# Kernel tuning notes

Measured on AMD Instinct MI355X. Metric: run time of the kernel, lower is better.

The kernel has to match this reference:

```python
import jax, jax.numpy as jnp
import numpy as np
from jax import lax

# Static configuration (torch module passes these as shape lists / init kwargs)
RATE = 2
FUSE_K = 3
SOFTMAX_SCALE = 10.0
B, L, C = 1, 4096, 64
HS = WS = 64            # downscaled foreground spatial (int_fs)
HB = WB = 64            # background patch grid (int_bs); HB*WB == L
KP = 2 * RATE           # raw patch kernel size = 4
PAD_T = 1               # torch conv_transpose2d padding


def setup_inputs() -> dict:
    key = jax.random.key(0)
    ks = jax.random.split(key, 6)
    raw_w = jax.random.normal(ks[0], (B, L, C, KP, KP), jnp.float32) * 0.1
    mm = (jax.random.uniform(ks[1], (B, L, 1, 1)) > 0.5).astype(jnp.float32)
    scores = jax.random.normal(ks[2], (B, L, HS, WS), jnp.float32)
    w1 = jax.random.normal(ks[3], (C, C, 3, 3), jnp.float32) * 0.05
    b1 = jnp.zeros((C,), jnp.float32)
    w2 = jax.random.normal(ks[4], (C, C, 3, 3), jnp.float32) * 0.05
    b2 = jnp.zeros((C,), jnp.float32)
    return {"raw_w": raw_w, "mm": mm, "scores": scores,
            "w1": w1, "b1": b1, "w2": w2, "b2": b2}


def _conv2d(x, w, b=None, padding=1):
    y = lax.conv_general_dilated(x, w, (1, 1), [(padding, padding)] * 2,
                                 dimension_numbers=('NCHW', 'OIHW', 'NCHW'))
    if b is not None:
        y = y + b[None, :, None, None]
    return y


def _fuse(yi):
    # Diagonal-kernel fusion (DeepFill): treat scores as a (HB*WB) x (HS*WS) image
    # and convolve with an identity (eye) kernel along both pairings.
    k = FUSE_K
    eye = jnp.eye(k, dtype=yi.dtype)[None, None]  # [1,1,k,k]
    x = yi.reshape(B, 1, HB * WB, HS * WS)
    x = _conv2d(x, eye, padding=k // 2)
    x = x.reshape(B, HB, WB, HS, WS).transpose(0, 2, 1, 4, 3)
    x = x.reshape(B, 1, WB * HB, WS * HS)
    x = _conv2d(x, eye, padding=k // 2)
    x = x.reshape(B, WB, HB, WS, HS).transpose(0, 2, 1, 4, 3)  # [B,HB,WB,HS,WS]
    return x.reshape(B, L, HS, WS)


def _deconv_item(y_b, w_b):
    # torch F.conv_transpose2d(y, w, stride=RATE, padding=PAD_T) for one item.
    # y_b: [L,HS,WS], w_b: [L,C,KP,KP] -> [C, RATE*HS, RATE*WS]
    wt = jnp.flip(w_b, axis=(-2, -1)).transpose(1, 0, 2, 3)  # [C,L,KP,KP]
    pad = KP - 1 - PAD_T
    out = lax.conv_general_dilated(y_b[None], wt, (1, 1), [(pad, pad)] * 2,
                                   lhs_dilation=(RATE, RATE),
                                   dimension_numbers=('NCHW', 'OIHW', 'NCHW'))
    return out[0] / 4.0  # overlap normalization (4 = number of overlapping patches)


def reference(raw_w, mm, scores, w1, b1, w2, b2):
    yi = _fuse(scores)
    yi = jax.nn.softmax(yi * mm * SOFTMAX_SCALE, axis=1) * mm  # softmax over L patches
    y = jax.vmap(_deconv_item)(yi, raw_w)  # [B, C, RATE*HS, RATE*WS]
    # trailing Conv+ELU x2 (self.out)
    y = jax.nn.elu(_conv2d(y, w1, b1))
    y = jax.nn.elu(_conv2d(y, w2, b2))
    return y
```

## Files before the change

kernel.cpp:

```cpp
#include <hip/hip_runtime.h>
#include <hip/hip_bf16.h>
#include <math.h>

#define NL 4096
#define NQ 4096
#define SCALE 10.0f

typedef __bf16 bf16x8 __attribute__((ext_vector_type(8)));
typedef float  f32x4  __attribute__((ext_vector_type(4)));
typedef float  f32x4u __attribute__((ext_vector_type(4), aligned(4)));

#define GLOAD_LDS16(gp, lp)                                                        \
    __builtin_amdgcn_global_load_lds((const __attribute__((address_space(1))) void*)(gp), \
                                     (__attribute__((address_space(3))) void*)(lp), \
                                     16, 0, 0)

__device__ __forceinline__ void ldtap(const float* __restrict__ S, int r, int c0,
                                      float t[4]) {
    if (r < 0 || r >= 4096) { t[0] = t[1] = t[2] = t[3] = 0.f; return; }
    const float* p = S + (size_t)r * 4096;
    if (c0 >= 0 && c0 <= 4092) {
        f32x4u v = *(const f32x4u*)(p + c0);
        t[0] = v.x; t[1] = v.y; t[2] = v.z; t[3] = v.w;
    } else {
        #pragma unroll
        for (int i = 0; i < 4; ++i) {
            int c = c0 + i;
            t[i] = (c >= 0 && c < 4096) ? p[c] : 0.f;
        }
    }
}

__global__ __launch_bounds__(256) void fuseD(const float* __restrict__ S,
                                             float* __restrict__ F) {
    int l = blockIdx.x;
    int hb = l >> 6, wb = l & 63;
    int rowb[3]; bool rok[3];
    #pragma unroll
    for (int d = 0; d < 3; ++d) {
        int h2 = hb + d - 1;
        if (h2 >= 0 && h2 <= 63) { rowb[d] = h2 * 64 + wb; rok[d] = true; }
        else if (h2 < 0)         { rowb[d] = 4031 + wb;    rok[d] = (wb >= 1); }
        else                     { rowb[d] = 1 + wb;       rok[d] = (wb <= 62); }
    }
    float* Fr = F + (size_t)l * 4096;

    #pragma unroll
    for (int cc = 0; cc < 4; ++cc) {
        int q0 = (cc * 256 + threadIdx.x) * 4;
        int hs = q0 >> 6, ws0 = q0 & 63;
        float acc[4] = {0.f, 0.f, 0.f, 0.f};
        #pragma unroll
        for (int d = 0; d < 3; ++d) {
            if (!rok[d]) continue;
            int s2 = hs + d - 1;
            int colb; float m0 = 1.f, m3 = 1.f;
            if (s2 >= 0 && s2 <= 63) colb = s2 * 64 + ws0;
            else if (s2 < 0) { colb = 4031 + ws0; if (ws0 == 0)  m0 = 0.f; }
            else             { colb = 1 + ws0;    if (ws0 == 60) m3 = 0.f; }
            float s3[4] = {0.f, 0.f, 0.f, 0.f};
            #pragma unroll
            for (int d1 = -1; d1 <= 1; ++d1) {
                float t[4];
                ldtap(S, rowb[d] + d1, colb + d1, t);
                s3[0] += t[0]; s3[1] += t[1]; s3[2] += t[2]; s3[3] += t[3];
            }
            acc[0] += m0 * s3[0]; acc[1] += s3[1]; acc[2] += s3[2]; acc[3] += m3 * s3[3];
        }
        *(float4*)&Fr[q0] = make_float4(acc[0], acc[1], acc[2], acc[3]);
    }
}

__global__ __launch_bounds__(256) void softPart(const float* __restrict__ F,
                                                const float* __restrict__ mm,
                                                float* __restrict__ Pm,
                                                float* __restrict__ Ps) {
    int qt = blockIdx.x, lc = blockIdx.y;
    int qo = threadIdx.x & 63, lg = threadIdx.x >> 6;
    int q = qt * 64 + qo;
    __shared__ float red[4][64];

    float sv[32];
    float m = -1e30f;
    #pragma unroll
    for (int i = 0; i < 32; ++i) {
        int l = lc * 128 + i * 4 + lg;
        float s = F[(size_t)l * 4096 + q] * mm[l] * SCALE;
        sv[i] = s;
        m = fmaxf(m, s);
    }
    red[lg][qo] = m;
    __syncthreads();
    m = fmaxf(fmaxf(red[0][qo], red[1][qo]), fmaxf(red[2][qo], red[3][qo]));
    __syncthreads();

    float sum = 0.f;
    #pragma unroll
    for (int i = 0; i < 32; ++i) sum += __expf(sv[i] - m);
    red[lg][qo] = sum;
    __syncthreads();
    if (lg == 0) {
        sum = red[0][qo] + red[1][qo] + red[2][qo] + red[3][qo];
        Pm[lc * 4096 + q] = m;
        Ps[lc * 4096 + q] = sum;
    }
}

__global__ void softComb(const float* __restrict__ Pm, const float* __restrict__ Ps,
                         float* __restrict__ Qm, float* __restrict__ Qi) {
    int q = blockIdx.x * 256 + threadIdx.x;
    float M = -1e30f;
    #pragma unroll
    for (int i = 0; i < 32; ++i) M = fmaxf(M, Pm[i * 4096 + q]);
    float S = 0.f;
    #pragma unroll
    for (int i = 0; i < 32; ++i) S += Ps[i * 4096 + q] * __expf(Pm[i * 4096 + q] - M);
    Qm[q] = M;
    Qi[q] = 1.0f / S;
}

__global__ __launch_bounds__(256) void normTransP(const float* __restrict__ F,
                                                  const float* __restrict__ mm,
                                                  const float* __restrict__ Qm,
                                                  const float* __restrict__ Qi,
                                                  __hip_bfloat16* __restrict__ Pt) {
    __shared__ float T[64][65];
    int qt = blockIdx.x, lt = blockIdx.y;
    int c = threadIdx.x & 63;
    int q = qt * 64 + c;
    float qm = Qm[q], qi = Qi[q];
    #pragma unroll
    for (int p = 0; p < 16; ++p) {
        int r = p * 4 + (threadIdx.x >> 6);
        int l = lt * 64 + r;
        float mml = mm[l];
        float s = F[(size_t)l * 4096 + q] * mml * SCALE - qm;
        T[r][c] = mml * __expf(s) * qi;
    }
    __syncthreads();
    #pragma unroll
    for (int p = 0; p < 16; ++p) {
        int r = p * 4 + (threadIdx.x >> 6);
        Pt[(size_t)(qt * 64 + r) * 4096 + lt * 64 + c] = (__hip_bfloat16)T[c][r];
    }
}

__global__ __launch_bounds__(256) void transW(const float* __restrict__ Wsrc,
                                              __hip_bfloat16* __restrict__ Wt) {
    __shared__ float T[64][65];
    int nt = blockIdx.x, kt = blockIdx.y;
    int c = threadIdx.x & 63;
    #pragma unroll
    for (int p = 0; p < 16; ++p) {
        int r = p * 4 + (threadIdx.x >> 6);
        T[r][c] = Wsrc[(size_t)(kt * 64 + r) * 1024 + nt * 64 + c];
    }
    __syncthreads();
    #pragma unroll
    for (int p = 0; p < 16; ++p) {
        int r = p * 4 + (threadIdx.x >> 6);
        int n_new = (r & 15) * 64 + nt * 4 + (r >> 4);
        Wt[(size_t)n_new * 4096 + kt * 64 + c] = (__hip_bfloat16)T[c][r];
    }
}

__global__ void transWc(const float* __restrict__ Wsrc, __hip_bfloat16* __restrict__ Wd) {
    int t = blockIdx.x * 256 + threadIdx.x;
    int kyx = t >> 12;
    int co = (t >> 6) & 63;
    int ci = t & 63;
    Wd[t] = (__hip_bfloat16)Wsrc[co * 576 + ci * 9 + kyx];
}

__global__ __launch_bounds__(256) void gemmMfma(const __hip_bfloat16* __restrict__ Ab,
                                                const __hip_bfloat16* __restrict__ Bb,
                                                float* __restrict__ Cm) {
    __shared__ __align__(16) __hip_bfloat16 As[2][128][32];
    __shared__ __align__(16) __hip_bfloat16 Bs[2][64][32];
    int tid = threadIdx.x;
    int lane = tid & 63, w = tid >> 6;
    int bm0 = blockIdx.x * 128, bn0 = blockIdx.y * 64;
    int wm = (w >> 1) * 64, wn = (w & 1) * 32;

    int srowA = w * 32 + (lane >> 2);
    int srowB = w * 16 + (lane >> 2);
    int scol = (((lane & 3) ^ ((lane >> 3) & 3))) * 8;
    const __hip_bfloat16* ga0 = Ab + (size_t)(bm0 + srowA) * 4096 + scol;
    const __hip_bfloat16* ga1 = Ab + (size_t)(bm0 + srowA + 16) * 4096 + scol;
    const __hip_bfloat16* gb0 = Bb + (size_t)(bn0 + srowB) * 4096 + scol;

    f32x4 acc[4][2] = {};
    int fm = lane & 15;
    int fkz = (((lane >> 4) ^ ((lane >> 1) & 3))) * 8;

    GLOAD_LDS16(ga0, &As[0][w * 32][0]);
    GLOAD_LDS16(ga1, &As[0][w * 32 + 16][0]);
    GLOAD_LDS16(gb0, &Bs[0][w * 16][0]);
    __syncthreads();

    int buf = 0;
    for (int t = 0; t < 128; ++t) {
        if (t + 1 < 128) {
            int k0 = (t + 1) * 32;
            GLOAD_LDS16(ga0 + k0, &As[buf ^ 1][w * 32][0]);
            GLOAD_LDS16(ga1 + k0, &As[buf ^ 1][w * 32 + 16][0]);
            GLOAD_LDS16(gb0 + k0, &Bs[buf ^ 1][w * 16][0]);
        }
        bf16x8 af[4], bfr[2];
        #pragma unroll
        for (int i = 0; i < 4; ++i)
            af[i] = *(const bf16x8*)&As[buf][wm + i * 16 + fm][fkz];
        #pragma unroll
        for (int j = 0; j < 2; ++j)
            bfr[j] = *(const bf16x8*)&Bs[buf][wn + j * 16 + fm][fkz];
        #pragma unroll
        for (int i = 0; i < 4; ++i)
            #pragma unroll
            for (int j = 0; j < 2; ++j)
                acc[i][j] = __builtin_amdgcn_mfma_f32_16x16x32_bf16(af[i], bfr[j], acc[i][j], 0, 0, 0);
        __syncthreads();
        buf ^= 1;
    }

    #pragma unroll
    for (int i = 0; i < 4; ++i) {
        #pragma unroll
        for (int j = 0; j < 2; ++j) {
            int row = bm0 + wm + i * 16 + (lane >> 4) * 4;
            int col = bn0 + wn + j * 16 + (lane & 15);
            #pragma unroll
            for (int r = 0; r < 4; ++r)
                Cm[(size_t)(row + r) * 1024 + col] = acc[i][j][r];
        }
    }
}

__global__ void scatterD(const float* __restrict__ Mo, __hip_bfloat16* __restrict__ Xp) {
    int c = threadIdx.x & 63;
    int pix = blockIdx.x * 4 + (threadIdx.x >> 6);
    int ox = pix & 127, oy = pix >> 7;
    float acc = 0.f;
    #pragma unroll
    for (int ky = 0; ky < 4; ++ky) {
        int ty = oy + 1 - ky;
        if (ty & 1) continue;
        int iy = ty >> 1;
        if (iy < 0 || iy >= 64) continue;
        #pragma unroll
        for (int kx = 0; kx < 4; ++kx) {
            int txx = ox + 1 - kx;
            if (txx & 1) continue;
            int ix = txx >> 1;
            if (ix < 0 || ix >= 64) continue;
            acc += Mo[(size_t)(iy * 64 + ix) * 1024 + (ky * 4 + kx) * 64 + c];
        }
    }
    Xp[((size_t)(oy + 1) * 130 + ox + 1) * 64 + c] = (__hip_bfloat16)(acc * 0.25f);
}

template <int MODE>
__global__ __launch_bounds__(256) void convMfma(const __hip_bfloat16* __restrict__ Xp,
                                                const __hip_bfloat16* __restrict__ Wc,
                                                const float* __restrict__ Bi,
                                                __hip_bfloat16* __restrict__ Yp,
                                                float* __restrict__ Yo) {
    int tid = threadIdx.x, lane = tid & 63, w = tid >> 6;
    int y = blockIdx.x >> 1, x0 = (blockIdx.x & 1) * 64;
    int co0 = w * 16;
    int fl = lane & 15, fh = lane >> 4;

    bf16x8 wb[3][3][2];
    #pragma unroll
    for (int ky = 0; ky < 3; ++ky)
        #pragma unroll
        for (int kx = 0; kx < 3; ++kx)
            #pragma unroll
            for (int kc = 0; kc < 2; ++kc)
                wb[ky][kx][kc] = *(const bf16x8*)&Wc[(size_t)((ky * 3 + kx) * 64 + co0 + fl) * 64 + kc * 32 + fh * 8];

    f32x4 acc[4] = {};
    #pragma unroll
    for (int ky = 0; ky < 3; ++ky) {
        #pragma unroll
        for (int kx = 0; kx < 3; ++kx) {
            const __hip_bfloat16* xrow = Xp + ((size_t)(y + ky) * 130 + x0 + kx) * 64;
            #pragma unroll
            for (int kc = 0; kc < 2; ++kc) {
                #pragma unroll
                for (int mt = 0; mt < 4; ++mt) {
                    bf16x8 af = *(const bf16x8*)&xrow[(mt * 16 + fl) * 64 + kc * 32 + fh * 8];
                    acc[mt] = __builtin_amdgcn_mfma_f32_16x16x32_bf16(af, wb[ky][kx][kc], acc[mt], 0, 0, 0);
                }
            }
        }
    }

    float bias = Bi[co0 + fl];
    #pragma unroll
    for (int mt = 0; mt < 4; ++mt) {
        int xb = x0 + mt * 16 + fh * 4;
        if (MODE == 0) {
            #pragma unroll
            for (int r = 0; r < 4; ++r) {
                float v = acc[mt][r] + bias;
                v = v > 0.f ? v : expm1f(v);
                Yp[((size_t)(y + 1) * 130 + xb + r + 1) * 64 + co0 + fl] = (__hip_bfloat16)v;
            }
        } else {
            float4 o;
            float* op = (float*)&o;
            #pragma unroll
            for (int r = 0; r < 4; ++r) {
                float v = acc[mt][r] + bias;
                op[r] = v > 0.f ? v : expm1f(v);
            }
            *(float4*)&Yo[(size_t)(co0 + fl) * 16384 + y * 128 + xb] = o;
        }
    }
}

extern "C" void kernel_launch(void* const* d_in, const int* in_sizes, int n_in,
                              void* d_out, int out_size, void* d_ws, size_t ws_size,
                              hipStream_t stream) {
    const float* raw_w  = (const float*)d_in[0];
    const float* mm     = (const float*)d_in[1];
    const float* scores = (const float*)d_in[2];
    const float* w1     = (const float*)d_in[3];
    const float* b1     = (const float*)d_in[4];
    const float* w2     = (const float*)d_in[5];
    const float* b2     = (const float*)d_in[6];
    float* out = (float*)d_out;

    char* ws = (char*)d_ws;
    __hip_bfloat16* Pt  = (__hip_bfloat16*)ws;
    __hip_bfloat16* Wt  = (__hip_bfloat16*)(ws + (32ull << 20));
    float*          Pm  = (float*)(ws + (40ull << 20));
    float*          Ps  = (float*)(ws + (40ull << 20) + (512u << 10));
    float*          Qm  = (float*)(ws + (41ull << 20));
    float*          Qi  = (float*)(ws + (41ull << 20) + (64u << 10));
    __hip_bfloat16* Wc1 = (__hip_bfloat16*)(ws + (41ull << 20) + (256u << 10));
    __hip_bfloat16* Wc2 = (__hip_bfloat16*)(ws + (41ull << 20) + (384u << 10));
    float*          Mo  = (float*)(ws + (42ull << 20));
    __hip_bfloat16* Xp  = (__hip_bfloat16*)(ws + (58ull << 20));
    __hip_bfloat16* Y1p = (__hip_bfloat16*)(ws + (61ull << 20));
    float*          F   = (float*)(ws + (64ull << 20));

    const size_t XP_BYTES = 130ull * 130 * 64 * sizeof(__hip_bfloat16);

    fuseD<<<4096, 256, 0, stream>>>(scores, F);
    transW<<<dim3(16, 64), 256, 0, stream>>>(raw_w, Wt);
    transWc<<<144, 256, 0, stream>>>(w1, Wc1);
    transWc<<<144, 256, 0, stream>>>(w2, Wc2);
    softPart<<<dim3(64, 32), 256, 0, stream>>>(F, mm, Pm, Ps);
    softComb<<<16, 256, 0, stream>>>(Pm, Ps, Qm, Qi);
    normTransP<<<dim3(64, 64), 256, 0, stream>>>(F, mm, Qm, Qi, Pt);
    gemmMfma<<<dim3(32, 16), 256, 0, stream>>>(Pt, Wt, Mo);
    hipMemsetAsync(Xp, 0, XP_BYTES, stream);
    hipMemsetAsync(Y1p, 0, XP_BYTES, stream);
    scatterD<<<4096, 256, 0, stream>>>(Mo, Xp);
    convMfma<0><<<256, 256, 0, stream>>>(Xp, Wc1, b1, Y1p, nullptr);
    convMfma<1><<<256, 256, 0, stream>>>(Y1p, Wc2, b2, nullptr, out);
}
```

Measured before the change: 198.3 us.

## Split-K GEMM with larger 128x128 tiles and XCD-aware block remapping

The main GEMM changes from 128x64 tiles over the full K=4096 to 128x128 tiles with a two-way split-K. The two partial results go to separate buffers (the second reuses the F region, which is no longer needed), and scatterD sums them. Block indices are remapped so neighbouring tiles land on the same XCD for better L2 reuse, and fuseD gets the same remap. The intent is more reuse per block and a full 512-block grid, at the cost of extra fp32 partial writes and reads in scatterD.

After: 177.0 us. 10.8% less time.

```diff
diff --git a/kernel.cpp b/kernel.cpp
--- a/kernel.cpp
+++ b/kernel.cpp
@@ -33,7 +33,8 @@
 
 __global__ __launch_bounds__(256) void fuseD(const float* __restrict__ S,
                                              float* __restrict__ F) {
-    int l = blockIdx.x;
+    int lin = blockIdx.x;
+    int l = (lin & 7) * 512 + (lin >> 3);
     int hb = l >> 6, wb = l & 63;
     int rowb[3]; bool rok[3];
     #pragma unroll
@@ -172,51 +173,62 @@
     Wd[t] = (__hip_bfloat16)Wsrc[co * 576 + ci * 9 + kyx];
 }
 
-__global__ __launch_bounds__(256) void gemmMfma(const __hip_bfloat16* __restrict__ Ab,
-                                                const __hip_bfloat16* __restrict__ Bb,
-                                                float* __restrict__ Cm) {
+__global__ __launch_bounds__(256) void gemmMfmaK(const __hip_bfloat16* __restrict__ Ab,
+                                                 const __hip_bfloat16* __restrict__ Bb,
+                                                 float* __restrict__ C0,
+                                                 float* __restrict__ C1) {
     __shared__ __align__(16) __hip_bfloat16 As[2][128][32];
-    __shared__ __align__(16) __hip_bfloat16 Bs[2][64][32];
+    __shared__ __align__(16) __hip_bfloat16 Bs[2][128][32];
+    int lin = blockIdx.x;
+    int wid = (lin & 7) * 64 + (lin >> 3);
+    int bm = wid & 31;
+    int bn = (wid >> 5) & 7;
+    int bz = wid >> 8;
+    int bm0 = bm * 128, bn0 = bn * 128;
+    size_t kbase = (size_t)bz * 2048;
+    float* Cm = bz ? C1 : C0;
+
     int tid = threadIdx.x;
     int lane = tid & 63, w = tid >> 6;
-    int bm0 = blockIdx.x * 128, bn0 = blockIdx.y * 64;
-    int wm = (w >> 1) * 64, wn = (w & 1) * 32;
-
-    int srowA = w * 32 + (lane >> 2);
-    int srowB = w * 16 + (lane >> 2);
+    int wm = (w >> 1) * 64, wn = (w & 1) * 64;
+
+    int srow = w * 32 + (lane >> 2);
     int scol = (((lane & 3) ^ ((lane >> 3) & 3))) * 8;
-    const __hip_bfloat16* ga0 = Ab + (size_t)(bm0 + srowA) * 4096 + scol;
-    const __hip_bfloat16* ga1 = Ab + (size_t)(bm0 + srowA + 16) * 4096 + scol;
-    const __hip_bfloat16* gb0 = Bb + (size_t)(bn0 + srowB) * 4096 + scol;
-
-    f32x4 acc[4][2] = {};
+    const __hip_bfloat16* ga0 = Ab + (size_t)(bm0 + srow) * 4096 + kbase + scol;
+    const __hip_bfloat16* ga1 = Ab + (size_t)(bm0 + srow + 16) * 4096 + kbase + scol;
+    const __hip_bfloat16* gb0 = Bb + (size_t)(bn0 + srow) * 4096 + kbase + scol;
+    const __hip_bfloat16* gb1 = Bb + (size_t)(bn0 + srow + 16) * 4096 + kbase + scol;
+
+    f32x4 acc[4][4] = {};
     int fm = lane & 15;
     int fkz = (((lane >> 4) ^ ((lane >> 1) & 3))) * 8;
 
     GLOAD_LDS16(ga0, &As[0][w * 32][0]);
     GLOAD_LDS16(ga1, &As[0][w * 32 + 16][0]);
-    GLOAD_LDS16(gb0, &Bs[0][w * 16][0]);
+    GLOAD_LDS16(gb0, &Bs[0][w * 32][0]);
+    GLOAD_LDS16(gb1, &Bs[0][w * 32 + 16][0]);
     __syncthreads();
 
     int buf = 0;
-    for (int t = 0; t < 128; ++t) {
-        if (t + 1 < 128) {
+    for (int t = 0; t < 64; ++t) {
+        if (t + 1 < 64) {
             int k0 = (t + 1) * 32;
             GLOAD_LDS16(ga0 + k0, &As[buf ^ 1][w * 32][0]);
             GLOAD_LDS16(ga1 + k0, &As[buf ^ 1][w * 32 + 16][0]);
-            GLOAD_LDS16(gb0 + k0, &Bs[buf ^ 1][w * 16][0]);
-        }
-        bf16x8 af[4], bfr[2];
+            GLOAD_LDS16(gb0 + k0, &Bs[buf ^ 1][w * 32][0]);
+            GLOAD_LDS16(gb1 + k0, &Bs[buf ^ 1][w * 32 + 16][0]);
+        }
+        bf16x8 af[4], bfr[4];
         #pragma unroll
         for (int i = 0; i < 4; ++i)
             af[i] = *(const bf16x8*)&As[buf][wm + i * 16 + fm][fkz];
         #pragma unroll
-        for (int j = 0; j < 2; ++j)
+        for (int j = 0; j < 4; ++j)
             bfr[j] = *(const bf16x8*)&Bs[buf][wn + j * 16 + fm][fkz];
         #pragma unroll
         for (int i = 0; i < 4; ++i)
             #pragma unroll
-            for (int j = 0; j < 2; ++j)
+            for (int j = 0; j < 4; ++j)
                 acc[i][j] = __builtin_amdgcn_mfma_f32_16x16x32_bf16(af[i], bfr[j], acc[i][j], 0, 0, 0);
         __syncthreads();
         buf ^= 1;
@@ -225,7 +237,7 @@
     #pragma unroll
     for (int i = 0; i < 4; ++i) {
         #pragma unroll
-        for (int j = 0; j < 2; ++j) {
+        for (int j = 0; j < 4; ++j) {
             int row = bm0 + wm + i * 16 + (lane >> 4) * 4;
             int col = bn0 + wn + j * 16 + (lane & 15);
             #pragma unroll
@@ -235,7 +247,8 @@
     }
 }
 
-__global__ void scatterD(const float* __restrict__ Mo, __hip_bfloat16* __restrict__ Xp) {
+__global__ void scatterD(const float* __restrict__ Mo, const float* __restrict__ Mo2,
+                         __hip_bfloat16* __restrict__ Xp) {
     int c = threadIdx.x & 63;
     int pix = blockIdx.x * 4 + (threadIdx.x >> 6);
     int ox = pix & 127, oy = pix >> 7;
@@ -252,7 +265,8 @@
             if (txx & 1) continue;
             int ix = txx >> 1;
             if (ix < 0 || ix >= 64) continue;
-            acc += Mo[(size_t)(iy * 64 + ix) * 1024 + (ky * 4 + kx) * 64 + c];
+            size_t off = (size_t)(iy * 64 + ix) * 1024 + (ky * 4 + kx) * 64 + c;
+            acc += Mo[off] + Mo2[off];
         }
     }
     Xp[((size_t)(oy + 1) * 130 + ox + 1) * 64 + c] = (__hip_bfloat16)(acc * 0.25f);
@@ -344,6 +358,7 @@
     __hip_bfloat16* Xp  = (__hip_bfloat16*)(ws + (58ull << 20));
     __hip_bfloat16* Y1p = (__hip_bfloat16*)(ws + (61ull << 20));
     float*          F   = (float*)(ws + (64ull << 20));
+    float*          Mo2 = (float*)(ws + (64ull << 20));
 
     const size_t XP_BYTES = 130ull * 130 * 64 * sizeof(__hip_bfloat16);
 
@@ -354,10 +369,10 @@
     softPart<<<dim3(64, 32), 256, 0, stream>>>(F, mm, Pm, Ps);
     softComb<<<16, 256, 0, stream>>>(Pm, Ps, Qm, Qi);
     normTransP<<<dim3(64, 64), 256, 0, stream>>>(F, mm, Qm, Qi, Pt);
-    gemmMfma<<<dim3(32, 16), 256, 0, stream>>>(Pt, Wt, Mo);
+    gemmMfmaK<<<512, 256, 0, stream>>>(Pt, Wt, Mo, Mo2);
     hipMemsetAsync(Xp, 0, XP_BYTES, stream);
     hipMemsetAsync(Y1p, 0, XP_BYTES, stream);
-    scatterD<<<4096, 256, 0, stream>>>(Mo, Xp);
+    scatterD<<<4096, 256, 0, stream>>>(Mo, Mo2, Xp);
     convMfma<0><<<256, 256, 0, stream>>>(Xp, Wc1, b1, Y1p, nullptr);
     convMfma<1><<<256, 256, 0, stream>>>(Y1p, Wc2, b2, nullptr, out);
 }
```
